# Kernel tuning notes

Measured on AMD Instinct MI355X. Metric: run time of the kernel, lower is better.

Reference implementation:

```python
import jax, jax.numpy as jnp
import numpy as np

N, K, S, E = 8192, 15, 128, 24
H, A, HID, DEPTH, MIX = 8, 32, 512, 3, 10
RBF_MAX, RBF_K = 20.0, 16


def _norm(v):
    return v / (jnp.linalg.norm(v, axis=-1, keepdims=True) + 1e-8)


def orientation_frames(pos):
    # pos: [N,3] CA coords -> per-residue local rotation frames [N,3,3]
    u = _norm(pos[1:] - pos[:-1])
    b = _norm(u[:-1] - u[1:])
    n = _norm(jnp.cross(u[:-1], u[1:]))
    o = jnp.cross(b, n)
    R = jnp.stack([b, n, o], axis=-1)              # [N-2,3,3]
    return jnp.concatenate([R[:1], R, R[-1:]], 0)  # edge-pad to [N,3,3]


def rot_to_quat(R):
    m00, m11, m22 = R[..., 0, 0], R[..., 1, 1], R[..., 2, 2]
    def comp(t, a, b):
        return 0.5 * jnp.sqrt(jnp.maximum(1e-8, t)) * jnp.sign(a - b)
    qw = 0.5 * jnp.sqrt(jnp.maximum(1e-8, 1. + m00 + m11 + m22))
    qx = comp(1. + m00 - m11 - m22, R[..., 2, 1], R[..., 1, 2])
    qy = comp(1. - m00 + m11 - m22, R[..., 0, 2], R[..., 2, 0])
    qz = comp(1. - m00 - m11 + m22, R[..., 1, 0], R[..., 0, 1])
    return jnp.stack([qw, qx, qy, qz], axis=-1)


def rbf_expand(d):
    mu = jnp.linspace(0., RBF_MAX, RBF_K)
    sigma = RBF_MAX / RBF_K
    return jnp.exp(-((d[..., None] - mu) / sigma) ** 2)


def layer_norm(x, g, b):
    m = x.mean(-1, keepdims=True)
    v = ((x - m) ** 2).mean(-1, keepdims=True)
    return (x - m) / jnp.sqrt(v + 1e-5) * g + b


def edge_features(pos, R, structure):
    # Target features are roll-by-1 of self (as in the torch forward's
    # distances.roll(1, dims=0)); sources are k-NN neighbours [N,K].
    inds = jnp.arange(N, dtype=pos.dtype)
    pos_t, R_t, ind_t = jnp.roll(pos, 1, 0), jnp.roll(R, 1, 0), jnp.roll(inds, 1, 0)
    pos_s, R_s, ind_s = pos[structure], R[structure], inds[structure]
    dvec = pos_s - pos_t[:, None]                    # [N,K,3]
    dist = jnp.linalg.norm(dvec, axis=-1)            # [N,K]
    direction = jnp.einsum('nji,nkj->nki', R_t, _norm(dvec))
    R_rel = jnp.einsum('nji,nkjl->nkil', R_t, R_s)   # R_t^T R_s
    quat = rot_to_quat(R_rel)                        # [N,K,4]
    rel_ind = (ind_s - ind_t[:, None])[..., None] / 100.0
    return jnp.concatenate([rbf_expand(dist), direction, quat, rel_ind], -1)  # [N,K,24]


def _forward(angles, tertiary, structure, W_in, b_in, W_pre, b_pre,
             ln1_g, ln1_b, Wq, bq, Wk, bk, Wv, bv, Wo, bo, ln2_g, ln2_b,
             W1, b1, W2, b2, W3, b3, Ws, bs, Wc, bc,
             W_conc, b_conc, W_wt, b_wt, W_fac, b_fac):
    prev = jnp.roll(angles, 1, 0).at[0].set(0.)
    afeat = jnp.concatenate([jnp.sin(prev), jnp.cos(prev)], -1)   # [N,6]
    feats = afeat @ W_in + b_in                                   # [N,S]
    pos = tertiary[:, 1]                                          # CA coords [N,3]
    R = orientation_frames(pos)
    edges = edge_features(pos, R, structure)                      # [N,K,E]
    x = feats @ W_pre + b_pre
    for d in range(DEPTH):
        nx = layer_norm(x, ln1_g[d], ln1_b[d])
        q = (nx @ Wq[d] + bq[d]).reshape(N, H, A)
        kv_in = jnp.concatenate([nx[structure], edges], -1)       # [N,K,S+E]
        k = (kv_in @ Wk[d] + bk[d]).reshape(N, K, H, A)
        v = (kv_in @ Wv[d] + bv[d]).reshape(N, K, H, A)
        logits = jnp.einsum('nha,nkha->nkh', q, k) / np.sqrt(A)
        attn = jax.nn.softmax(logits, axis=1)                     # over neighbours
        att = jnp.einsum('nkh,nkha->nha', attn, v).reshape(N, H * A) @ Wo[d] + bo[d]
        x = x + att
        h = layer_norm(x, ln2_g[d], ln2_b[d])
        h = jax.nn.relu(h @ W1[d] + b1[d])
        h = jax.nn.relu(h @ W2[d] + b2[d])
        x = x + (h @ W3[d] + b3[d])
    enc = x
    mean = jnp.arctan2(enc @ Ws + bs, enc @ Wc + bc).reshape(N, 3, MIX)
    factor = enc @ W_fac + b_fac
    mean = mean.at[:, 1].add((factor[:, 0] * angles[:, 0])[:, None])
    mean = mean.at[:, 2].add((factor[:, 1] * angles[:, 0] + factor[:, 2] * angles[:, 1])[:, None])
    conc = 0.1 + 1000. * jax.nn.sigmoid(enc @ W_conc + b_conc).reshape(N, 3, MIX)
    weights = jax.nn.softmax(enc @ W_wt + b_wt, axis=-1)
    return weights, mean, conc


def setup_inputs() -> dict:
    key = jax.random.key(0)
    ks = iter(jax.random.split(key, 64))
    def lin(i, o):
        return (jax.random.normal(next(ks), (i, o), jnp.float32) / np.sqrt(i),
                jnp.zeros((o,), jnp.float32))
    def stack_lin(i, o):
        w = jax.random.normal(next(ks), (DEPTH, i, o), jnp.float32) / np.sqrt(i)
        return w, jnp.zeros((DEPTH, o), jnp.float32)
    inp = {}
    inp['angles'] = jax.random.normal(next(ks), (N, 3), jnp.float32) * 1.5
    inp['tertiary'] = jax.random.normal(next(ks), (N, 3, 3), jnp.float32) * 3.0
    inp['structure'] = jax.random.randint(next(ks), (N, K), 0, N)
    inp['subgraph'] = jax.random.randint(next(ks), (N,), 0, 4)
    inp['W_in'], inp['b_in'] = lin(6, S)
    inp['W_pre'], inp['b_pre'] = lin(S, S)
    inp['ln1_g'] = jnp.ones((DEPTH, S)); inp['ln1_b'] = jnp.zeros((DEPTH, S))
    inp['ln2_g'] = jnp.ones((DEPTH, S)); inp['ln2_b'] = jnp.zeros((DEPTH, S))
    inp['Wq'], inp['bq'] = stack_lin(S, H * A)
    inp['Wk'], inp['bk'] = stack_lin(S + E, H * A)
    inp['Wv'], inp['bv'] = stack_lin(S + E, H * A)
    inp['Wo'], inp['bo'] = stack_lin(H * A, S)
    inp['W1'], inp['b1'] = stack_lin(S, HID)
    inp['W2'], inp['b2'] = stack_lin(HID, HID)
    inp['W3'], inp['b3'] = stack_lin(HID, S)
    inp['Ws'], inp['bs'] = lin(S, 3 * MIX)
    inp['Wc'], inp['bc'] = lin(S, 3 * MIX)
    inp['W_conc'], inp['b_conc'] = lin(S, 3 * MIX)
    inp['W_wt'], inp['b_wt'] = lin(S, MIX)
    inp['W_fac'], inp['b_fac'] = lin(S, 3)
    return inp


def reference(angles, tertiary, structure, subgraph, W_in, b_in, W_pre, b_pre,
              ln1_g, ln1_b, Wq, bq, Wk, bk, Wv, bv, Wo, bo, ln2_g, ln2_b,
              W1, b1, W2, b2, W3, b3, Ws, bs, Wc, bc,
              W_conc, b_conc, W_wt, b_wt, W_fac, b_fac):
    return _forward(angles, tertiary, structure, W_in, b_in, W_pre, b_pre,
                    ln1_g, ln1_b, Wq, bq, Wk, bk, Wv, bv, Wo, bo, ln2_g, ln2_b,
                    W1, b1, W2, b2, W3, b3, Ws, bs, Wc, bc,
                    W_conc, b_conc, W_wt, b_wt, W_fac, b_fac)
```

## Files before the change

### kernel.cpp

```cpp
#include <hip/hip_runtime.h>
#include <hip/hip_bf16.h>
#include <stdint.h>

#define NRES 8192
#define KNB  15
#define SDIM 128
#define EDIM 24
#define HIDD 512
#define NH   8
#define QDIM 256
#define MIXN 10

typedef _Float16 f16;
typedef _Float16 f16x8 __attribute__((ext_vector_type(8)));
typedef _Float16 f16x4 __attribute__((ext_vector_type(4)));
typedef _Float16 f16x2 __attribute__((ext_vector_type(2)));
typedef float f32x4 __attribute__((ext_vector_type(4)));

#if __has_builtin(__builtin_amdgcn_fdot2)
#define FDOT2(a,b,c) __builtin_amdgcn_fdot2((a),(b),(c),false)
#else
#define FDOT2(a,b,c) ((c) + (float)(a).x*(float)(b).x + (float)(a).y*(float)(b).y)
#endif

struct F3 { float x, y, z; };
__device__ __forceinline__ F3 f3sub(F3 a, F3 b) { return {a.x-b.x, a.y-b.y, a.z-b.z}; }
__device__ __forceinline__ F3 f3cross(F3 a, F3 b) {
  return {a.y*b.z - a.z*b.y, a.z*b.x - a.x*b.z, a.x*b.y - a.y*b.x};
}
__device__ __forceinline__ F3 f3norm(F3 a) {
  float l = sqrtf(a.x*a.x + a.y*a.y + a.z*a.z) + 1e-8f;
  float r = 1.f / l;
  return {a.x*r, a.y*r, a.z*r};
}
__device__ __forceinline__ F3 ldpos(const float* p, int i) { return {p[i*3], p[i*3+1], p[i*3+2]}; }

__global__ void pos_kernel(const float* __restrict__ tert, float* __restrict__ pos) {
  int n = blockIdx.x * blockDim.x + threadIdx.x;
  if (n >= NRES) return;
  pos[n*3+0] = tert[n*9+3];
  pos[n*3+1] = tert[n*9+4];
  pos[n*3+2] = tert[n*9+5];
}

__global__ void frames_kernel(const float* __restrict__ pos, float* __restrict__ R) {
  int m = blockIdx.x * blockDim.x + threadIdx.x;
  if (m >= NRES) return;
  int s = m - 1; if (s < 0) s = 0; if (s > NRES-3) s = NRES-3;
  F3 p0 = ldpos(pos, s), p1 = ldpos(pos, s+1), p2 = ldpos(pos, s+2);
  F3 u0 = f3norm(f3sub(p1, p0));
  F3 u1 = f3norm(f3sub(p2, p1));
  F3 b  = f3norm(f3sub(u0, u1));
  F3 nn = f3norm(f3cross(u0, u1));
  F3 o  = f3cross(b, nn);
  float* r = R + m*9;
  r[0]=b.x; r[1]=nn.x; r[2]=o.x;
  r[3]=b.y; r[4]=nn.y; r[5]=o.y;
  r[6]=b.z; r[7]=nn.z; r[8]=o.z;
}

__device__ __forceinline__ float quat_comp(float t, float a, float b) {
  float s = (a > b) ? 1.f : ((a < b) ? -1.f : 0.f);
  return 0.5f * sqrtf(fmaxf(1e-8f, t)) * s;
}

__global__ void edges_kernel(const float* __restrict__ pos, const float* __restrict__ R,
                             const int* __restrict__ structure, f16* __restrict__ edges) {
  int id = blockIdx.x * blockDim.x + threadIdx.x;
  if (id >= NRES*KNB) return;
  int n = id / KNB;
  int tprev = (n - 1) & (NRES - 1);
  int sidx = structure[id];
  F3 pt = ldpos(pos, tprev), ps = ldpos(pos, sidx);
  F3 dv = f3sub(ps, pt);
  float dist = sqrtf(dv.x*dv.x + dv.y*dv.y + dv.z*dv.z);
  float rinv = 1.f / (dist + 1e-8f);
  F3 dh = {dv.x*rinv, dv.y*rinv, dv.z*rinv};
  float Rt[9], Rs[9];
#pragma unroll
  for (int i = 0; i < 9; i++) { Rt[i] = R[tprev*9+i]; Rs[i] = R[sidx*9+i]; }
  float dir[3];
#pragma unroll
  for (int i = 0; i < 3; i++) dir[i] = Rt[i]*dh.x + Rt[3+i]*dh.y + Rt[6+i]*dh.z;
  float Rr[9];
#pragma unroll
  for (int i = 0; i < 3; i++)
#pragma unroll
    for (int l = 0; l < 3; l++)
      Rr[i*3+l] = Rt[i]*Rs[l] + Rt[3+i]*Rs[3+l] + Rt[6+i]*Rs[6+l];
  float m00 = Rr[0], m11 = Rr[4], m22 = Rr[8];
  float qw = 0.5f * sqrtf(fmaxf(1e-8f, 1.f + m00 + m11 + m22));
  float qx = quat_comp(1.f + m00 - m11 - m22, Rr[7], Rr[5]);
  float qy = quat_comp(1.f - m00 + m11 - m22, Rr[2], Rr[6]);
  float qz = quat_comp(1.f - m00 - m11 + m22, Rr[3], Rr[1]);
  f16* e = edges + (size_t)id * EDIM;
#pragma unroll
  for (int j = 0; j < 16; j++) {
    float mu = (20.f / 15.f) * j;
    float zz = (dist - mu) * (1.f / 1.25f);
    e[j] = (f16)expf(-zz*zz);
  }
  e[16] = (f16)dir[0]; e[17] = (f16)dir[1]; e[18] = (f16)dir[2];
  e[19] = (f16)qw; e[20] = (f16)qx; e[21] = (f16)qy; e[22] = (f16)qz;
  e[23] = (f16)((float)(sidx - tprev) * 0.01f);
}

__global__ __launch_bounds__(128) void init_kernel(const float* __restrict__ angles,
    const float* __restrict__ W_in, const float* __restrict__ b_in,
    const float* __restrict__ W_pre, const float* __restrict__ b_pre, float* __restrict__ x) {
  int n = blockIdx.x, c = threadIdx.x;
  __shared__ float fs[128];
  float af[6];
  if (n == 0) { af[0]=af[1]=af[2]=0.f; af[3]=af[4]=af[5]=1.f; }
  else {
#pragma unroll
    for (int j = 0; j < 3; j++) {
      float p = angles[(n-1)*3 + j];
      af[j] = sinf(p); af[3+j] = cosf(p);
    }
  }
  float f = b_in[c];
#pragma unroll
  for (int j = 0; j < 6; j++) f += af[j] * W_in[j*SDIM + c];
  fs[c] = f;
  __syncthreads();
  float xv = b_pre[c];
  for (int j = 0; j < 128; j++) xv += fs[j] * W_pre[j*SDIM + c];
  x[(size_t)n*SDIM + c] = xv;
}

__global__ __launch_bounds__(128) void ln_kernel(const float* __restrict__ x,
    const float* __restrict__ g, const float* __restrict__ b, f16* __restrict__ out) {
  int n = blockIdx.x, c = threadIdx.x;
  float v = x[(size_t)n*SDIM + c];
  float s = v;
#pragma unroll
  for (int m = 32; m >= 1; m >>= 1) s += __shfl_xor(s, m, 64);
  __shared__ float p1[2], p2[2];
  if ((c & 63) == 0) p1[c >> 6] = s;
  __syncthreads();
  float mean = (p1[0] + p1[1]) * (1.f/128.f);
  float d = v - mean;
  float s2 = d * d;
#pragma unroll
  for (int m = 32; m >= 1; m >>= 1) s2 += __shfl_xor(s2, m, 64);
  if ((c & 63) == 0) p2[c >> 6] = s2;
  __syncthreads();
  float var = (p2[0] + p2[1]) * (1.f/128.f);
  out[(size_t)n*SDIM + c] = (f16)(d * rsqrtf(var + 1e-5f) * g[c] + b[c]);
}

__global__ void convswz_kernel(const float* __restrict__ src, int srcLayerStride, int srcLd,
    int K, int N, f16* __restrict__ dst, int dstLayerHalves, int dstN, int colOff) {
  int d = blockIdx.y;
  const float* s = src + (size_t)d * srcLayerStride;
  f16* o = dst + (size_t)d * dstLayerHalves;
  for (int i = blockIdx.x*blockDim.x + threadIdx.x; i < K*N; i += gridDim.x*blockDim.x) {
    int k = i / N, n = i - k*N;
    o[((size_t)(k>>3)*dstN + colOff + n)*8 + (k&7)] = (f16)s[(size_t)k*srcLd + n];
  }
}

__global__ void wqdense_kernel(const float* __restrict__ Wk, const float* __restrict__ bk,
                               f16* __restrict__ dst) {
  int idx = blockIdx.x*blockDim.x + threadIdx.x;
  if (idx >= 3*256*256) return;
  int d = idx >> 16, r = (idx >> 8) & 255, col = idx & 255;
  float v = 0.f;
  if (col < 200) {
    int h = col / 25, jj = col % 25;
    if ((r >> 5) == h) {
      const float* WkB = Wk + (size_t)d*(SDIM+EDIM)*QDIM + (size_t)SDIM*QDIM;
      v = (jj < 24) ? WkB[(size_t)jj*QDIM + r] : bk[d*QDIM + r];
    }
  }
  dst[(size_t)d*65536 + ((size_t)(r>>3)*256 + col)*8 + (r&7)] = (f16)v;
}

__global__ void bias768_kernel(const float* __restrict__ bq, float* __restrict__ out) {
  int i = blockIdx.x*blockDim.x + threadIdx.x;
  if (i >= 3*768) return;
  int d = i / 768, col = i - d*768;
  out[i] = (col < 256) ? bq[d*QDIM + col] : 0.f;
}

template<int MODE>
__global__ __launch_bounds__(256) void gemm_mfma(const f16* __restrict__ A,
    const f16* __restrict__ Bsw, const float* __restrict__ bias,
    void* __restrict__ Cv, int Kd, int Nd) {
  int w = blockIdx.x * 4 + (threadIdx.x >> 6);
  int lane = threadIdx.x & 63;
  int wm = w & 255, wn = w >> 8;
  int m0 = wm * 32, n0 = wn * 64;
  int r16 = lane & 15, qd = lane >> 4;
  f32x4 acc[2][4] = {};
  const f16* aBase = A + (size_t)(m0 + r16)*Kd + qd*8;
  for (int kc = 0; kc < Kd; kc += 32) {
    f16x8 af0 = *(const f16x8*)(aBase + kc);
    f16x8 af1 = *(const f16x8*)(aBase + (size_t)16*Kd + kc);
    const f16* bBase = Bsw + ((size_t)((kc>>3) + qd)*Nd + n0 + r16)*8;
    f16x8 bf[4];
#pragma unroll
    for (int nt = 0; nt < 4; nt++) bf[nt] = *(const f16x8*)(bBase + nt*16*8);
#pragma unroll
    for (int nt = 0; nt < 4; nt++) {
      acc[0][nt] = __builtin_amdgcn_mfma_f32_16x16x32_f16(af0, bf[nt], acc[0][nt], 0, 0, 0);
      acc[1][nt] = __builtin_amdgcn_mfma_f32_16x16x32_f16(af1, bf[nt], acc[1][nt], 0, 0, 0);
    }
  }
#pragma unroll
  for (int mt = 0; mt < 2; mt++) {
#pragma unroll
    for (int nt = 0; nt < 4; nt++) {
      int col = n0 + nt*16 + r16;
      float bj = bias ? bias[col] : 0.f;
#pragma unroll
      for (int r = 0; r < 4; r++) {
        int row = m0 + mt*16 + qd*4 + r;
        float v = acc[mt][nt][r] + bj;
        if (MODE == 1) {
          ((f16*)Cv)[(size_t)row*Nd + col] = (f16)fmaxf(v, 0.f);
        } else if (MODE == 4) {
          ((float*)Cv)[(size_t)row*Nd + col] = v;
        } else {
          int third = col >> 8, cl = col & 255;
          ((f16*)Cv)[(size_t)third*NRES*QDIM + (size_t)row*QDIM + cl] = (f16)v;
        }
      }
    }
  }
}

__global__ __launch_bounds__(256) void gemm_mfma16(const f16* __restrict__ A,
    const f16* __restrict__ Bsw, const float* __restrict__ bias,
    float* __restrict__ C, int Kd, int Nd) {
  int w = blockIdx.x * 4 + (threadIdx.x >> 6);
  int lane = threadIdx.x & 63;
  int wm = w & 511, wn = w >> 9;
  int m0 = wm * 16, n0 = wn * 64;
  int r16 = lane & 15, qd = lane >> 4;
  f32x4 acc[4] = {};
  const f16* aBase = A + (size_t)(m0 + r16)*Kd + qd*8;
  for (int kc = 0; kc < Kd; kc += 32) {
    f16x8 af = *(const f16x8*)(aBase + kc);
    const f16* bBase = Bsw + ((size_t)((kc>>3) + qd)*Nd + n0 + r16)*8;
#pragma unroll
    for (int nt = 0; nt < 4; nt++) {
      f16x8 bf = *(const f16x8*)(bBase + nt*16*8);
      acc[nt] = __builtin_amdgcn_mfma_f32_16x16x32_f16(af, bf, acc[nt], 0, 0, 0);
    }
  }
#pragma unroll
  for (int nt = 0; nt < 4; nt++) {
    int col = n0 + nt*16 + r16;
    float bj = bias[col];
#pragma unroll
    for (int r = 0; r < 4; r++) {
      int row = m0 + qd*4 + r;
      C[(size_t)row*Nd + col] += acc[nt][r] + bj;
    }
  }
}

__global__ __launch_bounds__(256) void attn_kernel(const f16* __restrict__ q,
    const f16* __restrict__ pk, const f16* __restrict__ pv,
    const f16* __restrict__ edges, const int* __restrict__ structure,
    const float* __restrict__ qW, const float* __restrict__ WvB,
    const float* __restrict__ bv, f16* __restrict__ att) {
  int t = threadIdx.x;
  int n = blockIdx.x*4 + (t >> 6);
  int lane = t & 63;
  int h = lane >> 3, i = lane & 7, base = h << 3;

  int s[KNB];
#pragma unroll
  for (int kk = 0; kk < KNB; kk++) s[kk] = structure[n*KNB + kk];
  const f16x4* pk4 = (const f16x4*)pk;
  const f16x4* pv4 = (const f16x4*)pv;
  f16x4 pks[KNB], pvs[KNB];
#pragma unroll
  for (int kk = 0; kk < KNB; kk++) pks[kk] = pk4[(size_t)s[kk]*64 + lane];
#pragma unroll
  for (int kk = 0; kk < KNB; kk++) pvs[kk] = pv4[(size_t)s[kk]*64 + lane];
  f16x4 q4 = ((const f16x4*)q)[(size_t)n*64 + lane];

  const float* qwr = qW + (size_t)n*256 + h*25;
  float qbias = qwr[24];
  float elA = qbias, elB = qbias;
  {
    const f16x2* eA = (const f16x2*)(edges + (size_t)n*KNB*EDIM + i*EDIM);
#pragma unroll
    for (int j2 = 0; j2 < 12; j2++) {
      f16x2 e2 = eA[j2];
      elA += qwr[2*j2]*(float)e2.x + qwr[2*j2+1]*(float)e2.y;
    }
  }
  if (i < 7) {
    const f16x2* eB = (const f16x2*)(edges + (size_t)n*KNB*EDIM + (i+8)*EDIM);
#pragma unroll
    for (int j2 = 0; j2 < 12; j2++) {
      f16x2 e2 = eB[j2];
      elB += qwr[2*j2]*(float)e2.x + qwr[2*j2+1]*(float)e2.y;
    }
  }

  float dot[KNB];
  f16x2 qlo; qlo.x = q4.x; qlo.y = q4.y;
  f16x2 qhi; qhi.x = q4.z; qhi.y = q4.w;
#pragma unroll
  for (int kk = 0; kk < KNB; kk++) {
    f16x2 plo; plo.x = pks[kk].x; plo.y = pks[kk].y;
    f16x2 phi; phi.x = pks[kk].z; phi.y = pks[kk].w;
    float p = FDOT2(qlo, plo, 0.f);
    p = FDOT2(qhi, phi, p);
    p += __shfl_xor(p, 4, 64);
    p += __shfl_xor(p, 2, 64);
    p += __shfl_xor(p, 1, 64);
    dot[kk] = p;
  }

  float logit[KNB];
#pragma unroll
  for (int kk = 0; kk < 8; kk++) {
    float el = __shfl(elA, base + kk, 64);
    logit[kk] = (dot[kk] + el) * 0.17677669529663687f;
  }
#pragma unroll
  for (int kk = 8; kk < KNB; kk++) {
    float el = __shfl(elB, base + (kk - 8), 64);
    logit[kk] = (dot[kk] + el) * 0.17677669529663687f;
  }

  float mx = -1e30f;
#pragma unroll
  for (int kk = 0; kk < KNB; kk++) mx = fmaxf(mx, logit[kk]);
  float attw[KNB]; float sum = 0.f;
#pragma unroll
  for (int kk = 0; kk < KNB; kk++) { attw[kk] = expf(logit[kk] - mx); sum += attw[kk]; }
  float inv = 1.f / sum;
#pragma unroll
  for (int kk = 0; kk < KNB; kk++) attw[kk] *= inv;

  float4 o = ((const float4*)bv)[lane];
#pragma unroll
  for (int kk = 0; kk < KNB; kk++) {
    float a = attw[kk];
    o.x += a * (float)pvs[kk].x;
    o.y += a * (float)pvs[kk].y;
    o.z += a * (float)pvs[kk].z;
    o.w += a * (float)pvs[kk].w;
  }

  const f16* ebase = edges + (size_t)n*KNB*EDIM;
  float ew0 = 0.f, ew1 = 0.f, ew2 = 0.f;
#pragma unroll
  for (int kk = 0; kk < KNB; kk++) {
    float a = attw[kk];
    ew0 += a * (float)ebase[kk*EDIM + 3*i + 0];
    ew1 += a * (float)ebase[kk*EDIM + 3*i + 1];
    ew2 += a * (float)ebase[kk*EDIM + 3*i + 2];
  }

#pragma unroll
  for (int src = 0; src < 8; src++) {
    float w0 = __shfl(ew0, base + src, 64);
    float w1 = __shfl(ew1, base + src, 64);
    float w2 = __shfl(ew2, base + src, 64);
    float4 wv0 = ((const float4*)(WvB + (size_t)(3*src + 0)*QDIM))[lane];
    float4 wv1 = ((const float4*)(WvB + (size_t)(3*src + 1)*QDIM))[lane];
    float4 wv2 = ((const float4*)(WvB + (size_t)(3*src + 2)*QDIM))[lane];
    o.x += w0*wv0.x + w1*wv1.x + w2*wv2.x;
    o.y += w0*wv0.y + w1*wv1.y + w2*wv2.y;
    o.z += w0*wv0.z + w1*wv1.z + w2*wv2.z;
    o.w += w0*wv0.w + w1*wv1.w + w2*wv2.w;
  }

  f16x4 ov; ov.x = (f16)o.x; ov.y = (f16)o.y; ov.z = (f16)o.z; ov.w = (f16)o.w;
  ((f16x4*)att)[(size_t)n*64 + lane] = ov;
}

__global__ __launch_bounds__(128) void head_kernel(const float* __restrict__ enc,
    const float* Ws, const float* bs, const float* Wc, const float* bc,
    const float* Wconc, const float* bconc, const float* Wwt, const float* bwt,
    const float* Wfac, const float* bfac, const float* __restrict__ angles, float* __restrict__ out) {
  int n = blockIdx.x, t = threadIdx.x;
  __shared__ float es[128];
  __shared__ float outs[103];
  es[t] = enc[(size_t)n*SDIM + t];
  __syncthreads();
  const float* W = nullptr; const float* bb = nullptr; int col = 0, nc = 0;
  if (t < 30)       { W = Ws;    bb = bs;    col = t;       nc = 30; }
  else if (t < 60)  { W = Wc;    bb = bc;    col = t - 30;  nc = 30; }
  else if (t < 90)  { W = Wconc; bb = bconc; col = t - 60;  nc = 30; }
  else if (t < 100) { W = Wwt;   bb = bwt;   col = t - 90;  nc = 10; }
  else if (t < 103) { W = Wfac;  bb = bfac;  col = t - 100; nc = 3;  }
  if (W) {
    float acc = bb[col];
    for (int j = 0; j < 128; j++) acc += es[j] * W[j*nc + col];
    outs[t] = acc;
  }
  __syncthreads();
  if (t < MIXN) {
    float mx = -1e30f;
    for (int m = 0; m < MIXN; m++) mx = fmaxf(mx, outs[90 + m]);
    float sum = 0.f;
    for (int m = 0; m < MIXN; m++) sum += expf(outs[90 + m] - mx);
    out[(size_t)n*MIXN + t] = expf(outs[90 + t] - mx) / sum;
  }
  if (t < 30) {
    int j = t / 10;
    float v = atan2f(outs[t], outs[30 + t]);
    float a0 = angles[n*3 + 0], a1 = angles[n*3 + 1];
    if (j == 1) v += outs[100] * a0;
    if (j == 2) v += outs[101] * a0 + outs[102] * a1;
    out[(size_t)NRES*MIXN + (size_t)n*30 + t] = v;
    float z = outs[60 + t];
    float sg = 1.f / (1.f + expf(-z));
    out[(size_t)NRES*MIXN + (size_t)NRES*30 + (size_t)n*30 + t] = 0.1f + 1000.f * sg;
  }
}

extern "C" void kernel_launch(void* const* d_in, const int* in_sizes, int n_in,
                              void* d_out, int out_size, void* d_ws, size_t ws_size,
                              hipStream_t stream) {
  const float* angles   = (const float*)d_in[0];
  const float* tertiary = (const float*)d_in[1];
  const int*   structure = (const int*)d_in[2];
  const float* W_in  = (const float*)d_in[4];  const float* b_in  = (const float*)d_in[5];
  const float* W_pre = (const float*)d_in[6];  const float* b_pre = (const float*)d_in[7];
  const float* ln1_g = (const float*)d_in[8];  const float* ln1_b = (const float*)d_in[9];
  const float* ln2_g = (const float*)d_in[10]; const float* ln2_b = (const float*)d_in[11];
  const float* Wq = (const float*)d_in[12]; const float* bq = (const float*)d_in[13];
  const float* Wk = (const float*)d_in[14]; const float* bk = (const float*)d_in[15];
  const float* Wv = (const float*)d_in[16]; const float* bv = (const float*)d_in[17];
  const float* Wo = (const float*)d_in[18]; const float* bo = (const float*)d_in[19];
  const float* W1 = (const float*)d_in[20]; const float* b1 = (const float*)d_in[21];
  const float* W2 = (const float*)d_in[22]; const float* b2 = (const float*)d_in[23];
  const float* W3 = (const float*)d_in[24]; const float* b3 = (const float*)d_in[25];
  const float* Ws = (const float*)d_in[26]; const float* bs = (const float*)d_in[27];
  const float* Wc = (const float*)d_in[28]; const float* bc = (const float*)d_in[29];
  const float* Wconc = (const float*)d_in[30]; const float* bconc = (const float*)d_in[31];
  const float* Wwt = (const float*)d_in[32]; const float* bwt = (const float*)d_in[33];
  const float* Wfac = (const float*)d_in[34]; const float* bfac = (const float*)d_in[35];

  char* wsb = (char*)d_ws;
  float* pos   = (float*)(wsb + 0);
  float* Rm    = (float*)(wsb + 98304);
  f16*   edg_h = (f16*)  (wsb + 393216);
  float* x     = (float*)(wsb + 6291456);
  f16*   nx_h  = (f16*)  (wsb + 10485760);
  f16*   att_h = (f16*)  (wsb + 12582912);
  f16*   qh    = (f16*)  (wsb + 16777216);
  f16*   pkh   = (f16*)  (wsb + 20971520);
  f16*   pvh   = (f16*)  (wsb + 25165824);
  f16*   h1h   = (f16*)  (wsb + 29360128);
  f16*   h2h   = (f16*)  (wsb + 37748736);
  f16*   qkvw  = (f16*)  (wsb + 46137344);
  f16*   w1w   = (f16*)  (wsb + 46727168);
  f16*   w2w   = (f16*)  (wsb + 47120384);
  f16*   w3w   = (f16*)  (wsb + 48693248);
  f16*   wow   = (f16*)  (wsb + 49086464);
  float* b768  = (float*)(wsb + 49283072);
  float* qWb   = (float*)(wsb + 49292288);
  f16*   wqd   = (f16*)  (wsb + 57680896);

  pos_kernel<<<dim3((NRES+255)/256), dim3(256), 0, stream>>>(tertiary, pos);
  frames_kernel<<<dim3((NRES+255)/256), dim3(256), 0, stream>>>(pos, Rm);
  edges_kernel<<<dim3((NRES*KNB+255)/256), dim3(256), 0, stream>>>(pos, Rm, structure, edg_h);
  init_kernel<<<dim3(NRES), dim3(128), 0, stream>>>(angles, W_in, b_in, W_pre, b_pre, x);

  convswz_kernel<<<dim3(64,3), 256, 0, stream>>>(Wq, SDIM*QDIM, QDIM, 128, 256, qkvw, 98304, 768, 0);
  convswz_kernel<<<dim3(64,3), 256, 0, stream>>>(Wk, (SDIM+EDIM)*QDIM, QDIM, 128, 256, qkvw, 98304, 768, 256);
  convswz_kernel<<<dim3(64,3), 256, 0, stream>>>(Wv, (SDIM+EDIM)*QDIM, QDIM, 128, 256, qkvw, 98304, 768, 512);
  convswz_kernel<<<dim3(64,3), 256, 0, stream>>>(W1, SDIM*HIDD, HIDD, 128, 512, w1w, 65536, 512, 0);
  convswz_kernel<<<dim3(64,3), 256, 0, stream>>>(W2, HIDD*HIDD, HIDD, 512, 512, w2w, 262144, 512, 0);
  convswz_kernel<<<dim3(64,3), 256, 0, stream>>>(W3, HIDD*SDIM, SDIM, 512, 128, w3w, 65536, 128, 0);
  convswz_kernel<<<dim3(64,3), 256, 0, stream>>>(Wo, QDIM*SDIM, SDIM, 256, 128, wow, 32768, 128, 0);
  wqdense_kernel<<<768, 256, 0, stream>>>(Wk, bk, wqd);
  bias768_kernel<<<9, 256, 0, stream>>>(bq, b768);

  for (int d = 0; d < 3; ++d) {
    const float* WvD = Wv + (size_t)d*(SDIM+EDIM)*QDIM;
    ln_kernel<<<dim3(NRES), dim3(128), 0, stream>>>(x, ln1_g + d*SDIM, ln1_b + d*SDIM, nx_h);
    gemm_mfma<3><<<768, 256, 0, stream>>>(nx_h, qkvw + (size_t)d*98304, b768 + d*768, qh, 128, 768);
    gemm_mfma<4><<<256, 256, 0, stream>>>(qh, wqd + (size_t)d*65536, nullptr, qWb, 256, 256);
    attn_kernel<<<dim3(NRES/4), dim3(256), 0, stream>>>(qh, pkh, pvh, edg_h, structure,
        qWb, WvD + (size_t)SDIM*QDIM, bv + d*QDIM, att_h);
    gemm_mfma16<<<256, 256, 0, stream>>>(att_h, wow + (size_t)d*32768, bo + d*SDIM, x, 256, 128);
    ln_kernel<<<dim3(NRES), dim3(128), 0, stream>>>(x, ln2_g + d*SDIM, ln2_b + d*SDIM, nx_h);
    gemm_mfma<1><<<512, 256, 0, stream>>>(nx_h, w1w + (size_t)d*65536, b1 + d*HIDD, h1h, 128, 512);
    gemm_mfma<1><<<512, 256, 0, stream>>>(h1h, w2w + (size_t)d*262144, b2 + d*HIDD, h2h, 512, 512);
    gemm_mfma16<<<256, 256, 0, stream>>>(h2h, w3w + (size_t)d*65536, b3 + d*SDIM, x, 512, 128);
  }

  head_kernel<<<dim3(NRES), dim3(128), 0, stream>>>(x, Ws, bs, Wc, bc, Wconc, bconc,
      Wwt, bwt, Wfac, bfac, angles, (float*)d_out);
}
```

Measured before the change: 519.4 us.

## Fuse LayerNorm into QKV/FFN GEMMs and fold q·Wk projection into weights

Drops the standalone LayerNorm kernels. Each GEMM that consumes a normalized input now loads fp32 rows, computes mean and variance with shuffles, and builds the f16 MFMA operands in registers. The second GEMM that multiplied q by the dense edge-key matrix is removed. Its weight product Wq·WkB, with the matching bias, is precomputed once into extra columns 768–1023 of the QKV weight, so one GEMM writes both qkv and qWb. This saves kernel launches and the round trip of the intermediate through memory, at the cost of redundant per-row LN work across column tiles and a rounding change from precombining the weights.

```diff
diff --git a/kernel.cpp b/kernel.cpp
--- a/kernel.cpp
+++ b/kernel.cpp
@@ -129,27 +129,6 @@
   x[(size_t)n*SDIM + c] = xv;
 }
 
-__global__ __launch_bounds__(128) void ln_kernel(const float* __restrict__ x,
-    const float* __restrict__ g, const float* __restrict__ b, f16* __restrict__ out) {
-  int n = blockIdx.x, c = threadIdx.x;
-  float v = x[(size_t)n*SDIM + c];
-  float s = v;
-#pragma unroll
-  for (int m = 32; m >= 1; m >>= 1) s += __shfl_xor(s, m, 64);
-  __shared__ float p1[2], p2[2];
-  if ((c & 63) == 0) p1[c >> 6] = s;
-  __syncthreads();
-  float mean = (p1[0] + p1[1]) * (1.f/128.f);
-  float d = v - mean;
-  float s2 = d * d;
-#pragma unroll
-  for (int m = 32; m >= 1; m >>= 1) s2 += __shfl_xor(s2, m, 64);
-  if ((c & 63) == 0) p2[c >> 6] = s2;
-  __syncthreads();
-  float var = (p2[0] + p2[1]) * (1.f/128.f);
-  out[(size_t)n*SDIM + c] = (f16)(d * rsqrtf(var + 1e-5f) * g[c] + b[c]);
-}
-
 __global__ void convswz_kernel(const float* __restrict__ src, int srcLayerStride, int srcLd,
     int K, int N, f16* __restrict__ dst, int dstLayerHalves, int dstN, int colOff) {
   int d = blockIdx.y;
@@ -161,27 +140,34 @@
   }
 }
 
-__global__ void wqdense_kernel(const float* __restrict__ Wk, const float* __restrict__ bk,
-                               f16* __restrict__ dst) {
-  int idx = blockIdx.x*blockDim.x + threadIdx.x;
-  if (idx >= 3*256*256) return;
-  int d = idx >> 16, r = (idx >> 8) & 255, col = idx & 255;
-  float v = 0.f;
+__global__ __launch_bounds__(128) void wcomb_kernel(const float* __restrict__ Wq,
+    const float* __restrict__ bq, const float* __restrict__ Wk, const float* __restrict__ bk,
+    f16* __restrict__ qkvw, float* __restrict__ b1024) {
+  int blk = blockIdx.x;
+  int d = blk >> 8, col = blk & 255;
+  int k = threadIdx.x;
+  float acc = 0.f, bacc = 0.f;
   if (col < 200) {
     int h = col / 25, jj = col % 25;
-    if ((r >> 5) == h) {
-      const float* WkB = Wk + (size_t)d*(SDIM+EDIM)*QDIM + (size_t)SDIM*QDIM;
-      v = (jj < 24) ? WkB[(size_t)jj*QDIM + r] : bk[d*QDIM + r];
-    }
-  }
-  dst[(size_t)d*65536 + ((size_t)(r>>3)*256 + col)*8 + (r&7)] = (f16)v;
-}
-
-__global__ void bias768_kernel(const float* __restrict__ bq, float* __restrict__ out) {
+    const float* WkB = Wk + (size_t)d*(SDIM+EDIM)*QDIM + (size_t)SDIM*QDIM;
+    const float* wqrow = Wq + (size_t)d*SDIM*QDIM + (size_t)k*QDIM;
+    int r0 = h*32;
+    for (int rr = 0; rr < 32; rr++) {
+      int r = r0 + rr;
+      float wd = (jj < 24) ? WkB[(size_t)jj*QDIM + r] : bk[d*QDIM + r];
+      acc += wqrow[r] * wd;
+      if (k == 0) bacc += bq[d*QDIM + r] * wd;
+    }
+  }
+  qkvw[(size_t)d*131072 + ((size_t)(k>>3)*1024 + 768 + col)*8 + (k&7)] = (f16)acc;
+  if (k == 0) b1024[d*1024 + 768 + col] = bacc;
+}
+
+__global__ void bias1024_kernel(const float* __restrict__ bq, float* __restrict__ out) {
   int i = blockIdx.x*blockDim.x + threadIdx.x;
   if (i >= 3*768) return;
   int d = i / 768, col = i - d*768;
-  out[i] = (col < 256) ? bq[d*QDIM + col] : 0.f;
+  out[d*1024 + col] = (col < 256) ? bq[d*QDIM + col] : 0.f;
 }
 
 template<int MODE>
@@ -218,13 +204,110 @@
       for (int r = 0; r < 4; r++) {
         int row = m0 + mt*16 + qd*4 + r;
         float v = acc[mt][nt][r] + bj;
+        ((f16*)Cv)[(size_t)row*Nd + col] = (f16)fmaxf(v, 0.f);
+      }
+    }
+  }
+}
+
+template<int MODE>
+__global__ __launch_bounds__(256) void gemm_ln_mfma(const float* __restrict__ A,
+    const float* __restrict__ lng, const float* __restrict__ lnb,
+    const f16* __restrict__ Bsw, const float* __restrict__ bias,
+    void* __restrict__ Cv, float* __restrict__ C2, int Nd) {
+  int w = blockIdx.x * 4 + (threadIdx.x >> 6);
+  int lane = threadIdx.x & 63;
+  int wm = w & 255, wn = w >> 8;
+  int m0 = wm * 32, n0 = wn * 64;
+  int r16 = lane & 15, qd = lane >> 4;
+  const float* r0p = A + (size_t)(m0 + r16)*SDIM + qd*8;
+  const float* r1p = r0p + (size_t)16*SDIM;
+  float4 a0[8], a1[8];
+#pragma unroll
+  for (int kc = 0; kc < 4; kc++) {
+    a0[kc*2+0] = *(const float4*)(r0p + kc*32);
+    a0[kc*2+1] = *(const float4*)(r0p + kc*32 + 4);
+    a1[kc*2+0] = *(const float4*)(r1p + kc*32);
+    a1[kc*2+1] = *(const float4*)(r1p + kc*32 + 4);
+  }
+  float s0 = 0.f, s1 = 0.f;
+#pragma unroll
+  for (int c = 0; c < 8; c++) {
+    s0 += a0[c].x + a0[c].y + a0[c].z + a0[c].w;
+    s1 += a1[c].x + a1[c].y + a1[c].z + a1[c].w;
+  }
+  s0 += __shfl_xor(s0, 16, 64); s0 += __shfl_xor(s0, 32, 64);
+  s1 += __shfl_xor(s1, 16, 64); s1 += __shfl_xor(s1, 32, 64);
+  float mean0 = s0 * (1.f/128.f), mean1 = s1 * (1.f/128.f);
+  float v0 = 0.f, v1 = 0.f;
+#pragma unroll
+  for (int c = 0; c < 8; c++) {
+    float d0x = a0[c].x-mean0, d0y = a0[c].y-mean0, d0z = a0[c].z-mean0, d0w = a0[c].w-mean0;
+    v0 += d0x*d0x + d0y*d0y + d0z*d0z + d0w*d0w;
+    float d1x = a1[c].x-mean1, d1y = a1[c].y-mean1, d1z = a1[c].z-mean1, d1w = a1[c].w-mean1;
+    v1 += d1x*d1x + d1y*d1y + d1z*d1z + d1w*d1w;
+  }
+  v0 += __shfl_xor(v0, 16, 64); v0 += __shfl_xor(v0, 32, 64);
+  v1 += __shfl_xor(v1, 16, 64); v1 += __shfl_xor(v1, 32, 64);
+  float rs0 = rsqrtf(v0 * (1.f/128.f) + 1e-5f);
+  float rs1 = rsqrtf(v1 * (1.f/128.f) + 1e-5f);
+  f16x8 af0[4], af1[4];
+#pragma unroll
+  for (int kc = 0; kc < 4; kc++) {
+    float4 g0 = *(const float4*)(lng + qd*8 + kc*32);
+    float4 g1 = *(const float4*)(lng + qd*8 + kc*32 + 4);
+    float4 bl0 = *(const float4*)(lnb + qd*8 + kc*32);
+    float4 bl1 = *(const float4*)(lnb + qd*8 + kc*32 + 4);
+    f16x8 f0, f1;
+    f0[0] = (f16)((a0[kc*2].x  -mean0)*rs0*g0.x + bl0.x);
+    f0[1] = (f16)((a0[kc*2].y  -mean0)*rs0*g0.y + bl0.y);
+    f0[2] = (f16)((a0[kc*2].z  -mean0)*rs0*g0.z + bl0.z);
+    f0[3] = (f16)((a0[kc*2].w  -mean0)*rs0*g0.w + bl0.w);
+    f0[4] = (f16)((a0[kc*2+1].x-mean0)*rs0*g1.x + bl1.x);
+    f0[5] = (f16)((a0[kc*2+1].y-mean0)*rs0*g1.y + bl1.y);
+    f0[6] = (f16)((a0[kc*2+1].z-mean0)*rs0*g1.z + bl1.z);
+    f0[7] = (f16)((a0[kc*2+1].w-mean0)*rs0*g1.w + bl1.w);
+    f1[0] = (f16)((a1[kc*2].x  -mean1)*rs1*g0.x + bl0.x);
+    f1[1] = (f16)((a1[kc*2].y  -mean1)*rs1*g0.y + bl0.y);
+    f1[2] = (f16)((a1[kc*2].z  -mean1)*rs1*g0.z + bl0.z);
+    f1[3] = (f16)((a1[kc*2].w  -mean1)*rs1*g0.w + bl0.w);
+    f1[4] = (f16)((a1[kc*2+1].x-mean1)*rs1*g1.x + bl1.x);
+    f1[5] = (f16)((a1[kc*2+1].y-mean1)*rs1*g1.y + bl1.y);
+    f1[6] = (f16)((a1[kc*2+1].z-mean1)*rs1*g1.z + bl1.z);
+    f1[7] = (f16)((a1[kc*2+1].w-mean1)*rs1*g1.w + bl1.w);
+    af0[kc] = f0; af1[kc] = f1;
+  }
+  f32x4 acc[2][4] = {};
+#pragma unroll
+  for (int kc = 0; kc < 4; kc++) {
+    const f16* bBase = Bsw + ((size_t)(kc*4 + qd)*Nd + n0 + r16)*8;
+    f16x8 bf[4];
+#pragma unroll
+    for (int nt = 0; nt < 4; nt++) bf[nt] = *(const f16x8*)(bBase + nt*16*8);
+#pragma unroll
+    for (int nt = 0; nt < 4; nt++) {
+      acc[0][nt] = __builtin_amdgcn_mfma_f32_16x16x32_f16(af0[kc], bf[nt], acc[0][nt], 0, 0, 0);
+      acc[1][nt] = __builtin_amdgcn_mfma_f32_16x16x32_f16(af1[kc], bf[nt], acc[1][nt], 0, 0, 0);
+    }
+  }
+#pragma unroll
+  for (int mt = 0; mt < 2; mt++) {
+#pragma unroll
+    for (int nt = 0; nt < 4; nt++) {
+      int col = n0 + nt*16 + r16;
+      float bj = bias[col];
+#pragma unroll
+      for (int r = 0; r < 4; r++) {
+        int row = m0 + mt*16 + qd*4 + r;
+        float v = acc[mt][nt][r] + bj;
         if (MODE == 1) {
           ((f16*)Cv)[(size_t)row*Nd + col] = (f16)fmaxf(v, 0.f);
-        } else if (MODE == 4) {
-          ((float*)Cv)[(size_t)row*Nd + col] = v;
         } else {
           int third = col >> 8, cl = col & 255;
-          ((f16*)Cv)[(size_t)third*NRES*QDIM + (size_t)row*QDIM + cl] = (f16)v;
+          if (third < 3)
+            ((f16*)Cv)[(size_t)third*NRES*QDIM + (size_t)row*QDIM + cl] = (f16)v;
+          else
+            C2[(size_t)row*256 + cl] = v;
         }
       }
     }
@@ -448,7 +531,6 @@
   float* Rm    = (float*)(wsb + 98304);
   f16*   edg_h = (f16*)  (wsb + 393216);
   float* x     = (float*)(wsb + 6291456);
-  f16*   nx_h  = (f16*)  (wsb + 10485760);
   f16*   att_h = (f16*)  (wsb + 12582912);
   f16*   qh    = (f16*)  (wsb + 16777216);
   f16*   pkh   = (f16*)  (wsb + 20971520);
@@ -456,39 +538,37 @@
   f16*   h1h   = (f16*)  (wsb + 29360128);
   f16*   h2h   = (f16*)  (wsb + 37748736);
   f16*   qkvw  = (f16*)  (wsb + 46137344);
-  f16*   w1w   = (f16*)  (wsb + 46727168);
-  f16*   w2w   = (f16*)  (wsb + 47120384);
-  f16*   w3w   = (f16*)  (wsb + 48693248);
-  f16*   wow   = (f16*)  (wsb + 49086464);
-  float* b768  = (float*)(wsb + 49283072);
-  float* qWb   = (float*)(wsb + 49292288);
-  f16*   wqd   = (f16*)  (wsb + 57680896);
+  f16*   w1w   = (f16*)  (wsb + 46923776);
+  f16*   w2w   = (f16*)  (wsb + 47316992);
+  f16*   w3w   = (f16*)  (wsb + 48889856);
+  f16*   wow   = (f16*)  (wsb + 49283072);
+  float* b1024 = (float*)(wsb + 49479680);
+  float* qWb   = (float*)(wsb + 49491968);
 
   pos_kernel<<<dim3((NRES+255)/256), dim3(256), 0, stream>>>(tertiary, pos);
   frames_kernel<<<dim3((NRES+255)/256), dim3(256), 0, stream>>>(pos, Rm);
   edges_kernel<<<dim3((NRES*KNB+255)/256), dim3(256), 0, stream>>>(pos, Rm, structure, edg_h);
   init_kernel<<<dim3(NRES), dim3(128), 0, stream>>>(angles, W_in, b_in, W_pre, b_pre, x);
 
-  convswz_kernel<<<dim3(64,3), 256, 0, stream>>>(Wq, SDIM*QDIM, QDIM, 128, 256, qkvw, 98304, 768, 0);
-  convswz_kernel<<<dim3(64,3), 256, 0, stream>>>(Wk, (SDIM+EDIM)*QDIM, QDIM, 128, 256, qkvw, 98304, 768, 256);
-  convswz_kernel<<<dim3(64,3), 256, 0, stream>>>(Wv, (SDIM+EDIM)*QDIM, QDIM, 128, 256, qkvw, 98304, 768, 512);
+  convswz_kernel<<<dim3(64,3), 256, 0, stream>>>(Wq, SDIM*QDIM, QDIM, 128, 256, qkvw, 131072, 1024, 0);
+  convswz_kernel<<<dim3(64,3), 256, 0, stream>>>(Wk, (SDIM+EDIM)*QDIM, QDIM, 128, 256, qkvw, 131072, 1024, 256);
+  convswz_kernel<<<dim3(64,3), 256, 0, stream>>>(Wv, (SDIM+EDIM)*QDIM, QDIM, 128, 256, qkvw, 131072, 1024, 512);
   convswz_kernel<<<dim3(64,3), 256, 0, stream>>>(W1, SDIM*HIDD, HIDD, 128, 512, w1w, 65536, 512, 0);
   convswz_kernel<<<dim3(64,3), 256, 0, stream>>>(W2, HIDD*HIDD, HIDD, 512, 512, w2w, 262144, 512, 0);
   convswz_kernel<<<dim3(64,3), 256, 0, stream>>>(W3, HIDD*SDIM, SDIM, 512, 128, w3w, 65536, 128, 0);
   convswz_kernel<<<dim3(64,3), 256, 0, stream>>>(Wo, QDIM*SDIM, SDIM, 256, 128, wow, 32768, 128, 0);
-  wqdense_kernel<<<768, 256, 0, stream>>>(Wk, bk, wqd);
-  bias768_kernel<<<9, 256, 0, stream>>>(bq, b768);
+  wcomb_kernel<<<768, 128, 0, stream>>>(Wq, bq, Wk, bk, qkvw, b1024);
+  bias1024_kernel<<<9, 256, 0, stream>>>(bq, b1024);
 
   for (int d = 0; d < 3; ++d) {
     const float* WvD = Wv + (size_t)d*(SDIM+EDIM)*QDIM;
-    ln_kernel<<<dim3(NRES), dim3(128), 0, stream>>>(x, ln1_g + d*SDIM, ln1_b + d*SDIM, nx_h);
-    gemm_mfma<3><<<768, 256, 0, stream>>>(nx_h, qkvw + (size_t)d*98304, b768 + d*768, qh, 128, 768);
-    gemm_mfma<4><<<256, 256, 0, stream>>>(qh, wqd + (size_t)d*65536, nullptr, qWb, 256, 256);
+    gemm_ln_mfma<3><<<1024, 256, 0, stream>>>(x, ln1_g + d*SDIM, ln1_b + d*SDIM,
+        qkvw + (size_t)d*131072, b1024 + d*1024, qh, qWb, 1024);
     attn_kernel<<<dim3(NRES/4), dim3(256), 0, stream>>>(qh, pkh, pvh, edg_h, structure,
         qWb, WvD + (size_t)SDIM*QDIM, bv + d*QDIM, att_h);
     gemm_mfma16<<<256, 256, 0, stream>>>(att_h, wow + (size_t)d*32768, bo + d*SDIM, x, 256, 128);
-    ln_kernel<<<dim3(NRES), dim3(128), 0, stream>>>(x, ln2_g + d*SDIM, ln2_b + d*SDIM, nx_h);
-    gemm_mfma<1><<<512, 256, 0, stream>>>(nx_h, w1w + (size_t)d*65536, b1 + d*HIDD, h1h, 128, 512);
+    gemm_ln_mfma<1><<<512, 256, 0, stream>>>(x, ln2_g + d*SDIM, ln2_b + d*SDIM,
+        w1w + (size_t)d*65536, b1 + d*HIDD, h1h, nullptr, 512);
     gemm_mfma<1><<<512, 256, 0, stream>>>(h1h, w2w + (size_t)d*262144, b2 + d*HIDD, h2h, 512, 512);
     gemm_mfma16<<<256, 256, 0, stream>>>(h2h, w3w + (size_t)d*65536, b3 + d*SDIM, x, 512, 128);
   }
```

New measurement: 504.7 us. 2.8% less time.
